# Performance work log

Measured on AMD Instinct MI355X. Metric: run time of the kernel, lower is better.

Reference implementation:

```python
import jax, jax.numpy as jnp
import numpy as np

L, E, H, FF, N, S, ML = 6, 768, 12, 3072, 8, 1023, 2048


def setup_inputs() -> dict:
    key = jax.random.key(0)
    ks = jax.random.split(key, 16)
    rn = lambda k, shape, s=0.02: jax.random.normal(k, shape, jnp.float32) * s
    return {
        "x": jax.random.normal(ks[0], (N, S, E), jnp.float32),
        "mask": jnp.ones((N, 1, 1, S + 1), jnp.int32),
        "pos_emb": rn(ks[1], (ML, E), 1.0),
        "cls": rn(ks[2], (1, 1, E), 1.0),
        "Wq": rn(ks[3], (L, E, E)), "bq": jnp.zeros((L, E), jnp.float32),
        "Wk": rn(ks[4], (L, E, E)), "bk": jnp.zeros((L, E), jnp.float32),
        "Wv": rn(ks[5], (L, E, E)), "bv": jnp.zeros((L, E), jnp.float32),
        "Wo": rn(ks[6], (L, E, E)), "bo": jnp.zeros((L, E), jnp.float32),
        "ln1_g": jnp.ones((L, E), jnp.float32), "ln1_b": jnp.zeros((L, E), jnp.float32),
        "ln2_g": jnp.ones((L, E), jnp.float32), "ln2_b": jnp.zeros((L, E), jnp.float32),
        "Wf1": rn(ks[7], (L, E, FF)), "bf1": jnp.zeros((L, FF), jnp.float32),
        "Wf2": rn(ks[8], (L, FF, E)), "bf2": jnp.zeros((L, E), jnp.float32),
    }


def _ln(x, g, b, eps=1e-5):
    m = x.mean(-1, keepdims=True)
    v = ((x - m) ** 2).mean(-1, keepdims=True)
    return (x - m) / jnp.sqrt(v + eps) * g + b


def reference(x, mask, pos_emb, cls, Wq, bq, Wk, bk, Wv, bv, Wo, bo,
              ln1_g, ln1_b, ln2_g, ln2_b, Wf1, bf1, Wf2, bf2):
    n, s, e = x.shape
    h = H
    d = e // h
    # prepend CLS token -> [N, T, E], add learned positions
    x = jnp.concatenate([jnp.broadcast_to(cls, (n, 1, e)), x], axis=1)
    t = s + 1
    out = x + pos_emb[:t][None]
    scale = jnp.float32(1.0 / np.sqrt(d))
    for i in range(Wq.shape[0]):
        q = (out @ Wq[i] + bq[i]).reshape(n, t, h, d)
        k = (out @ Wk[i] + bk[i]).reshape(n, t, h, d)
        v = (out @ Wv[i] + bv[i]).reshape(n, t, h, d)
        energy = jnp.einsum('nqhd,nkhd->nhqk', q, k)  # [N,H,T,T]
        energy = jnp.where(mask == 0, jnp.float32(-1e20), energy)
        attn = jax.nn.softmax(energy * scale, axis=-1)
        att = jnp.einsum('nhqk,nkhd->nqhd', attn, v).reshape(n, t, e)
        att = att @ Wo[i] + bo[i]
        hid = _ln(att + out, ln1_g[i], ln1_b[i])  # residual uses query (=out)
        ff = jax.nn.gelu(hid @ Wf1[i] + bf1[i], approximate=False) @ Wf2[i] + bf2[i]
        out = _ln(ff + hid, ln2_g[i], ln2_b[i])
    return out
```

## Files before the change

### kernel.cpp

```cpp
#include <hip/hip_runtime.h>

#define L_ 6
#define E_ 768
#define H_ 12
#define FF_ 3072

typedef __attribute__((ext_vector_type(8))) short bh8;
typedef __attribute__((ext_vector_type(4))) float f32x4;

__device__ inline ushort f2bf(float f) {
  unsigned u = __builtin_bit_cast(unsigned, f);
  u += 0x7fffu + ((u >> 16) & 1u);
  return (ushort)(u >> 16);
}

__device__ __forceinline__ void gload16(const void* g, void* l) {
  __builtin_amdgcn_global_load_lds(
      (const __attribute__((address_space(1))) void*)g,
      (__attribute__((address_space(3))) void*)l, 16, 0, 0);
}

__global__ __launch_bounds__(256) void pack_bias(const float* __restrict__ bq,
                                                 const float* __restrict__ bk,
                                                 const float* __restrict__ bv,
                                                 float* __restrict__ bqkv) {
  int idx = blockIdx.x * 256 + threadIdx.x;
  int l = idx / 2304, j = idx % 2304;
  float v = (j < 768) ? bq[l * 768 + j]
          : (j < 1536) ? bk[l * 768 + j - 768]
                       : bv[l * 768 + j - 1536];
  bqkv[idx] = v;
}

__global__ __launch_bounds__(256) void transpose_w(const float* __restrict__ src,
                                                   ushort* __restrict__ dst,
                                                   int K, int Nn,
                                                   long sstride, long dstride) {
  src += (long)blockIdx.z * sstride;
  dst += (long)blockIdx.z * dstride;
  __shared__ float t[32][33];
  int tx = threadIdx.x & 31, ty = threadIdx.x >> 5;
  int kb = blockIdx.x * 32, nb = blockIdx.y * 32;
#pragma unroll
  for (int i = 0; i < 4; i++) {
    int kr = ty + i * 8;
    t[kr][tx] = src[(long)(kb + kr) * Nn + nb + tx];
  }
  __syncthreads();
#pragma unroll
  for (int i = 0; i < 4; i++) {
    int nr = ty + i * 8;
    dst[(long)(nb + nr) * K + kb + tx] = f2bf(t[tx][nr]);
  }
}

__global__ __launch_bounds__(256) void embed_k(const float* __restrict__ x,
                                               const float* __restrict__ pos,
                                               const float* __restrict__ cls,
                                               float* __restrict__ res,
                                               ushort* __restrict__ xb) {
  int idx = blockIdx.x * 256 + threadIdx.x;
  int c4 = idx % 192;
  int row = idx / 192;
  int t = row & 1023, n = row >> 10;
  f32x4 pv = ((const f32x4*)pos)[t * 192 + c4];
  f32x4 xv;
  if (t == 0) xv = ((const f32x4*)cls)[c4];
  else        xv = ((const f32x4*)x)[(size_t)(n * 1023 + t - 1) * 192 + c4];
  f32x4 s = xv + pv;
  ((f32x4*)res)[idx] = s;
  ushort4 h;
  h.x = f2bf(s[0]); h.y = f2bf(s[1]); h.z = f2bf(s[2]); h.w = f2bf(s[3]);
  ((ushort4*)xb)[idx] = h;
}

template <int MODE>
__global__ __launch_bounds__(256) void gemm_bt(const ushort* __restrict__ A,
                                               const ushort* __restrict__ Bt,
                                               int M, int N, int K,
                                               const float* __restrict__ bias,
                                               const float* __restrict__ resid,
                                               float* __restrict__ out32,
                                               ushort* __restrict__ out16,
                                               ushort* __restrict__ vtb) {
  __shared__ ushort As[3][128 * 32];
  __shared__ ushort Bs[3][128 * 32];
  int tid = threadIdx.x;
  int wid = tid >> 6, lane = tid & 63;
  int wm = wid >> 1, wn = wid & 1;
  int l15 = lane & 15, lhi = lane >> 4;
  int ln4 = lane >> 2;
  int swc = (((lane & 3) ^ (ln4 & 3)) << 3);
  int xsl = ((lhi ^ (l15 & 3)) << 3);
  int row0 = blockIdx.x * 128, col0 = blockIdx.y * 128;

  f32x4 acc[4][4];
#pragma unroll
  for (int i = 0; i < 4; i++)
#pragma unroll
    for (int j = 0; j < 4; j++) acc[i][j] = (f32x4){0.f, 0.f, 0.f, 0.f};

  const ushort* Ab = A + (size_t)(row0 + wid * 32 + ln4) * K + swc;
  const ushort* Bb = Bt + (size_t)(col0 + wid * 32 + ln4) * K + swc;

  auto stage = [&](int b, int kt) {
#pragma unroll
    for (int it = 0; it < 2; ++it) {
      int r = wid * 32 + it * 16;
      gload16(Ab + (size_t)it * 16 * K + kt * 32, &As[b][r * 32]);
      gload16(Bb + (size_t)it * 16 * K + kt * 32, &Bs[b][r * 32]);
    }
  };

  int nt = K >> 5;
  stage(0, 0);
  stage(1, 1);
  int b0 = 0;
  for (int kt = 0; kt < nt; ++kt) {
    int rem = nt - kt;
    if (rem > 2) {
      stage((b0 + 2 >= 3) ? b0 - 1 : b0 + 2, kt + 2);
      asm volatile("s_waitcnt vmcnt(8)" ::: "memory");
    } else if (rem == 2) {
      asm volatile("s_waitcnt vmcnt(4)" ::: "memory");
    } else {
      asm volatile("s_waitcnt vmcnt(0)" ::: "memory");
    }
    __builtin_amdgcn_s_barrier();

    bh8 af[4], bfr[4];
#pragma unroll
    for (int i = 0; i < 4; i++)
      af[i] = *(const bh8*)(&As[b0][(wm * 64 + i * 16 + l15) * 32 + xsl]);
#pragma unroll
    for (int j = 0; j < 4; j++)
      bfr[j] = *(const bh8*)(&Bs[b0][(wn * 64 + j * 16 + l15) * 32 + xsl]);
#pragma unroll
    for (int i = 0; i < 4; i++)
#pragma unroll
      for (int j = 0; j < 4; j++)
        acc[i][j] = __builtin_amdgcn_mfma_f32_16x16x32_bf16(af[i], bfr[j], acc[i][j], 0, 0, 0);

    if (rem > 1) {
      asm volatile("s_waitcnt lgkmcnt(0)" ::: "memory");
      __builtin_amdgcn_s_barrier();
    }
    b0 = (b0 + 1 == 3) ? 0 : b0 + 1;
  }

#pragma unroll
  for (int j = 0; j < 4; j++) {
    int col = col0 + wn * 64 + j * 16 + l15;
    float bv = bias[col];
#pragma unroll
    for (int i = 0; i < 4; i++) {
      int rbase = row0 + wm * 64 + i * 16 + lhi * 4;
      if (MODE == 0 && col >= 1536) {
        int hd = col - 1536;
        int nn = rbase >> 10, t0 = rbase & 1023;
        ushort4 h4;
        h4.x = f2bf(acc[i][j][0] + bv);
        h4.y = f2bf(acc[i][j][1] + bv);
        h4.z = f2bf(acc[i][j][2] + bv);
        h4.w = f2bf(acc[i][j][3] + bv);
        *(ushort4*)(vtb + ((size_t)nn * 768 + hd) * 1024 + t0) = h4;
      } else {
#pragma unroll
        for (int r = 0; r < 4; r++) {
          int row = rbase + r;
          size_t o = (size_t)row * N + col;
          float v = acc[i][j][r] + bv;
          if (MODE == 0) {
            out16[o] = f2bf(v);
          } else if (MODE == 1) {
            out32[o] = v + resid[o];
          } else {
            v = 0.5f * v * (1.f + erff(v * 0.70710678118f));
            out16[o] = f2bf(v);
          }
        }
      }
    }
  }
}

__global__ __launch_bounds__(256) void attn_k(const ushort* __restrict__ qkv,
                                              const ushort* __restrict__ vtb,
                                              const int* __restrict__ mask,
                                              ushort* __restrict__ attb) {
  int qt = blockIdx.x, h = blockIdx.y, n = blockIdx.z;
  int tid = threadIdx.x, wid = tid >> 6, lane = tid & 63;
  int l15 = lane & 15, lhi = lane >> 4;
  __shared__ ushort Ks[2][64 * 64];
  __shared__ ushort Vs[2][64 * 64];
  __shared__ ushort Pt[4][16 * 64];
  ushort* Pw = Pt[wid];

  int ln8 = lane >> 3;
  int swc = (((lane & 7) ^ ln8) << 3);

  const ushort* Kg = qkv + 768 + h * 64;
  const ushort* Vg = vtb + (size_t)(n * 768 + h * 64) * 1024;

  auto stage = [&](int b, int kv0) {
#pragma unroll
    for (int it = 0; it < 2; ++it) {
      int r = wid * 16 + it * 8;
      gload16(Kg + (size_t)(n * 1024 + kv0 + r + ln8) * 2304 + swc, &Ks[b][r * 64]);
      gload16(Vg + (size_t)(r + ln8) * 1024 + kv0 + swc, &Vs[b][r * 64]);
    }
  };

  stage(0, 0);

  int q0 = qt * 64 + wid * 16;
  size_t rowQ = (size_t)(n * 1024 + q0 + l15) * 2304 + h * 64;
  bh8 qf0 = *(const bh8*)(qkv + rowQ + lhi * 8);
  bh8 qf1 = *(const bh8*)(qkv + rowQ + 32 + lhi * 8);

  unsigned long long mbits = 0ull;
#pragma unroll
  for (int i = 0; i < 64; ++i)
    mbits |= (unsigned long long)(mask[n * 1024 + i * 16 + l15] != 0) << i;

  bh8 ones;
#pragma unroll
  for (int i = 0; i < 8; ++i) ones[i] = (short)0x3F80;

  f32x4 o[4], lacc = (f32x4){0.f, 0.f, 0.f, 0.f};
#pragma unroll
  for (int i = 0; i < 4; i++) o[i] = (f32x4){0.f, 0.f, 0.f, 0.f};

  int x15 = (l15 & 7) << 3;
  int buf = 0;
  for (int t = 0; t < 16; ++t) {
    if (t < 15) {
      stage(buf ^ 1, (t + 1) * 64);
      asm volatile("s_waitcnt vmcnt(4)" ::: "memory");
    } else {
      asm volatile("s_waitcnt vmcnt(0)" ::: "memory");
    }
    __builtin_amdgcn_s_barrier();
    const ushort* Kb = Ks[buf];
    const ushort* Vb = Vs[buf];

    f32x4 s[4];
    __builtin_amdgcn_s_setprio(1);
#pragma unroll
    for (int t4 = 0; t4 < 4; ++t4) {
      int rs = (t4 * 16 + l15) * 64;
      s[t4] = (f32x4){0.f, 0.f, 0.f, 0.f};
      s[t4] = __builtin_amdgcn_mfma_f32_16x16x32_bf16(qf0, *(const bh8*)(Kb + rs + ((lhi << 3) ^ x15)), s[t4], 0, 0, 0);
      s[t4] = __builtin_amdgcn_mfma_f32_16x16x32_bf16(qf1, *(const bh8*)(Kb + rs + (((4 + lhi) << 3) ^ x15)), s[t4], 0, 0, 0);
    }
    __builtin_amdgcn_s_setprio(0);

#pragma unroll
    for (int t4 = 0; t4 < 4; ++t4) {
      bool mk = (mbits >> (t * 4 + t4)) & 1ull;
#pragma unroll
      for (int r = 0; r < 4; r++) {
        float xv = mk ? s[t4][r] * 0.125f : -1e20f;
        float p = __expf(fminf(xv, 80.f));
        int prow = lhi * 4 + r;
        int slot = t4 * 2 + (l15 >> 3);
        Pw[prow * 64 + (((slot ^ (prow & 7)) << 3) | (l15 & 7))] = f2bf(p);
      }
    }

    bh8 pf0 = *(const bh8*)(Pw + l15 * 64 + ((lhi << 3) ^ x15));
    bh8 pf1 = *(const bh8*)(Pw + l15 * 64 + (((4 + lhi) << 3) ^ x15));
    __builtin_amdgcn_s_setprio(1);
#pragma unroll
    for (int nb = 0; nb < 4; nb++) {
      int rs = (nb * 16 + l15) * 64;
      o[nb] = __builtin_amdgcn_mfma_f32_16x16x32_bf16(pf0, *(const bh8*)(Vb + rs + ((lhi << 3) ^ x15)), o[nb], 0, 0, 0);
      o[nb] = __builtin_amdgcn_mfma_f32_16x16x32_bf16(pf1, *(const bh8*)(Vb + rs + (((4 + lhi) << 3) ^ x15)), o[nb], 0, 0, 0);
    }
    lacc = __builtin_amdgcn_mfma_f32_16x16x32_bf16(pf0, ones, lacc, 0, 0, 0);
    lacc = __builtin_amdgcn_mfma_f32_16x16x32_bf16(pf1, ones, lacc, 0, 0, 0);
    __builtin_amdgcn_s_setprio(0);

    if (t < 15) {
      asm volatile("s_waitcnt lgkmcnt(0)" ::: "memory");
      __builtin_amdgcn_s_barrier();
    }
    buf ^= 1;
  }

#pragma unroll
  for (int nb = 0; nb < 4; nb++)
#pragma unroll
    for (int r = 0; r < 4; r++) {
      float val = o[nb][r] / lacc[r];
      int row = q0 + lhi * 4 + r;
      int col = h * 64 + nb * 16 + l15;
      attb[(size_t)(n * 1024 + row) * 768 + col] = f2bf(val);
    }
}

__global__ __launch_bounds__(256) void ln_k(const float* __restrict__ in,
                                            const float* __restrict__ g,
                                            const float* __restrict__ b,
                                            float* __restrict__ y32,
                                            ushort* __restrict__ y16) {
  int row = blockIdx.x, tid = threadIdx.x;
  size_t base = (size_t)row * 768;
  float v0 = in[base + tid], v1 = in[base + tid + 256], v2 = in[base + tid + 512];
  float s = v0 + v1 + v2;
  float sq = v0 * v0 + v1 * v1 + v2 * v2;
#pragma unroll
  for (int off = 32; off > 0; off >>= 1) {
    s += __shfl_down(s, off);
    sq += __shfl_down(sq, off);
  }
  __shared__ float sws[4], swq[4];
  int wid = tid >> 6, lane = tid & 63;
  if (lane == 0) { sws[wid] = s; swq[wid] = sq; }
  __syncthreads();
  float ts = sws[0] + sws[1] + sws[2] + sws[3];
  float tq = swq[0] + swq[1] + swq[2] + swq[3];
  float mean = ts * (1.f / 768.f);
  float var = tq * (1.f / 768.f) - mean * mean;
  float rstd = rsqrtf(var + 1e-5f);
#pragma unroll
  for (int i = 0; i < 3; i++) {
    int c = tid + i * 256;
    float vv = (i == 0) ? v0 : (i == 1) ? v1 : v2;
    float y = (vv - mean) * rstd * g[c] + b[c];
    y32[base + c] = y;
    y16[base + c] = f2bf(y);
  }
}

extern "C" void kernel_launch(void* const* d_in, const int* in_sizes, int n_in,
                              void* d_out, int out_size, void* d_ws, size_t ws_size,
                              hipStream_t stream) {
  const float* x    = (const float*)d_in[0];
  const int*   mask = (const int*)d_in[1];
  const float* pos  = (const float*)d_in[2];
  const float* cls  = (const float*)d_in[3];
  const float* Wq   = (const float*)d_in[4];
  const float* bq   = (const float*)d_in[5];
  const float* Wk   = (const float*)d_in[6];
  const float* bk   = (const float*)d_in[7];
  const float* Wv   = (const float*)d_in[8];
  const float* bv   = (const float*)d_in[9];
  const float* Wo   = (const float*)d_in[10];
  const float* bo   = (const float*)d_in[11];
  const float* ln1g = (const float*)d_in[12];
  const float* ln1b = (const float*)d_in[13];
  const float* ln2g = (const float*)d_in[14];
  const float* ln2b = (const float*)d_in[15];
  const float* Wf1  = (const float*)d_in[16];
  const float* bf1  = (const float*)d_in[17];
  const float* Wf2  = (const float*)d_in[18];
  const float* bf2  = (const float*)d_in[19];

  char* ws = (char*)d_ws;
  size_t off = 0;
  auto alloc = [&](size_t bytes) {
    char* p = ws + off;
    off += (bytes + 255) & ~(size_t)255;
    return p;
  };
  const size_t M = 8192;
  ushort* qkvt = (ushort*)alloc((size_t)L_ * 2304 * 768 * 2);
  ushort* wot  = (ushort*)alloc((size_t)L_ * 768 * 768 * 2);
  ushort* wf1t = (ushort*)alloc((size_t)L_ * 3072 * 768 * 2);
  ushort* wf2t = (ushort*)alloc((size_t)L_ * 768 * 3072 * 2);
  float*  bqkv = (float*)alloc((size_t)L_ * 2304 * 4);
  float*  res  = (float*)alloc(M * 768 * 4);
  float*  pre  = (float*)alloc(M * 768 * 4);
  ushort* xb   = (ushort*)alloc(M * 768 * 2);
  ushort* qkvb = (ushort*)alloc(M * 2304 * 2);
  ushort* vtb  = (ushort*)alloc(M * 768 * 2);
  ushort* attb = (ushort*)alloc(M * 768 * 2);
  ushort* ffb  = (ushort*)alloc(M * 3072 * 2);
  (void)ws_size; (void)in_sizes; (void)n_in; (void)out_size;

  dim3 tb(256);
  pack_bias<<<54, tb, 0, stream>>>(bq, bk, bv, bqkv);
  transpose_w<<<dim3(24, 24, 6), tb, 0, stream>>>(Wq, qkvt,              768, 768, 768L * 768, 2304L * 768);
  transpose_w<<<dim3(24, 24, 6), tb, 0, stream>>>(Wk, qkvt + 768 * 768,  768, 768, 768L * 768, 2304L * 768);
  transpose_w<<<dim3(24, 24, 6), tb, 0, stream>>>(Wv, qkvt + 2 * 768 * 768, 768, 768, 768L * 768, 2304L * 768);
  transpose_w<<<dim3(24, 24, 6), tb, 0, stream>>>(Wo, wot, 768, 768, 768L * 768, 768L * 768);
  transpose_w<<<dim3(24, 96, 6), tb, 0, stream>>>(Wf1, wf1t, 768, 3072, 768L * 3072, 3072L * 768);
  transpose_w<<<dim3(96, 24, 6), tb, 0, stream>>>(Wf2, wf2t, 3072, 768, 3072L * 768, 768L * 3072);
  embed_k<<<6144, tb, 0, stream>>>(x, pos, cls, res, xb);

  for (int l = 0; l < L_; l++) {
    gemm_bt<0><<<dim3(64, 18), tb, 0, stream>>>(xb, qkvt + (size_t)l * 2304 * 768,
                                                8192, 2304, 768, bqkv + l * 2304,
                                                nullptr, nullptr, qkvb, vtb);
    attn_k<<<dim3(16, 12, 8), tb, 0, stream>>>(qkvb, vtb, mask, attb);
    gemm_bt<1><<<dim3(64, 6), tb, 0, stream>>>(attb, wot + (size_t)l * 768 * 768,
                                               8192, 768, 768, bo + l * 768,
                                               res, pre, nullptr, nullptr);
    ln_k<<<8192, tb, 0, stream>>>(pre, ln1g + l * 768, ln1b + l * 768, res, xb);
    gemm_bt<2><<<dim3(64, 24), tb, 0, stream>>>(xb, wf1t + (size_t)l * 3072 * 768,
                                                8192, 3072, 768, bf1 + l * 3072,
                                                nullptr, nullptr, ffb, nullptr);
    gemm_bt<1><<<dim3(64, 6), tb, 0, stream>>>(ffb, wf2t + (size_t)l * 768 * 3072,
                                               8192, 768, 3072, bf2 + l * 768,
                                               res, pre, nullptr, nullptr);
    float* y32 = (l == L_ - 1) ? (float*)d_out : res;
    ln_k<<<8192, tb, 0, stream>>>(pre, ln2g + l * 768, ln2b + l * 768, y32, xb);
  }
}
```

Measured before the change: 1.976 ms.

## Replace triple-buffered GEMM pipeline with single-buffer BK=64 loop and higher occupancy

The GEMM main loop drops its 3-stage software-pipelined LDS ring with manual vmcnt waits. It now uses a single LDS buffer with K-tile 64, loads and computes each tile synchronously between __syncthreads, and sets launch_bounds to 4 blocks per CU. The XOR swizzle on LDS addresses is removed. Latency hiding now depends on occupancy instead of in-block prefetch. The unswizzled 128-byte row stride may cause LDS bank conflicts on the fragment reads.

```diff
diff --git a/kernel.cpp b/kernel.cpp
--- a/kernel.cpp
+++ b/kernel.cpp
@@ -75,23 +75,21 @@
 }
 
 template <int MODE>
-__global__ __launch_bounds__(256) void gemm_bt(const ushort* __restrict__ A,
-                                               const ushort* __restrict__ Bt,
-                                               int M, int N, int K,
-                                               const float* __restrict__ bias,
-                                               const float* __restrict__ resid,
-                                               float* __restrict__ out32,
-                                               ushort* __restrict__ out16,
-                                               ushort* __restrict__ vtb) {
-  __shared__ ushort As[3][128 * 32];
-  __shared__ ushort Bs[3][128 * 32];
+__global__ __launch_bounds__(256, 4) void gemm_bt(const ushort* __restrict__ A,
+                                                  const ushort* __restrict__ Bt,
+                                                  int M, int N, int K,
+                                                  const float* __restrict__ bias,
+                                                  const float* __restrict__ resid,
+                                                  float* __restrict__ out32,
+                                                  ushort* __restrict__ out16,
+                                                  ushort* __restrict__ vtb) {
+  __shared__ ushort As[128 * 64];
+  __shared__ ushort Bs[128 * 64];
   int tid = threadIdx.x;
   int wid = tid >> 6, lane = tid & 63;
   int wm = wid >> 1, wn = wid & 1;
   int l15 = lane & 15, lhi = lane >> 4;
-  int ln4 = lane >> 2;
-  int swc = (((lane & 3) ^ (ln4 & 3)) << 3);
-  int xsl = ((lhi ^ (l15 & 3)) << 3);
+  int ln8 = lane >> 3, lc8 = (lane & 7) * 8;
   int row0 = blockIdx.x * 128, col0 = blockIdx.y * 128;
 
   f32x4 acc[4][4];
@@ -100,52 +98,35 @@
 #pragma unroll
     for (int j = 0; j < 4; j++) acc[i][j] = (f32x4){0.f, 0.f, 0.f, 0.f};
 
-  const ushort* Ab = A + (size_t)(row0 + wid * 32 + ln4) * K + swc;
-  const ushort* Bb = Bt + (size_t)(col0 + wid * 32 + ln4) * K + swc;
-
-  auto stage = [&](int b, int kt) {
-#pragma unroll
-    for (int it = 0; it < 2; ++it) {
-      int r = wid * 32 + it * 16;
-      gload16(Ab + (size_t)it * 16 * K + kt * 32, &As[b][r * 32]);
-      gload16(Bb + (size_t)it * 16 * K + kt * 32, &Bs[b][r * 32]);
-    }
-  };
-
-  int nt = K >> 5;
-  stage(0, 0);
-  stage(1, 1);
-  int b0 = 0;
+  const ushort* Ap = A + (size_t)(row0 + wid * 32 + ln8) * K + lc8;
+  const ushort* Bp = Bt + (size_t)(col0 + wid * 32 + ln8) * K + lc8;
+
+  int nt = K >> 6;
   for (int kt = 0; kt < nt; ++kt) {
-    int rem = nt - kt;
-    if (rem > 2) {
-      stage((b0 + 2 >= 3) ? b0 - 1 : b0 + 2, kt + 2);
-      asm volatile("s_waitcnt vmcnt(8)" ::: "memory");
-    } else if (rem == 2) {
-      asm volatile("s_waitcnt vmcnt(4)" ::: "memory");
-    } else {
-      asm volatile("s_waitcnt vmcnt(0)" ::: "memory");
-    }
-    __builtin_amdgcn_s_barrier();
-
-    bh8 af[4], bfr[4];
-#pragma unroll
-    for (int i = 0; i < 4; i++)
-      af[i] = *(const bh8*)(&As[b0][(wm * 64 + i * 16 + l15) * 32 + xsl]);
-#pragma unroll
-    for (int j = 0; j < 4; j++)
-      bfr[j] = *(const bh8*)(&Bs[b0][(wn * 64 + j * 16 + l15) * 32 + xsl]);
-#pragma unroll
-    for (int i = 0; i < 4; i++)
+    int k0 = kt << 6;
+#pragma unroll
+    for (int p = 0; p < 4; p++) {
+      int r = wid * 32 + p * 8;
+      gload16(Ap + (size_t)p * 8 * K + k0, As + r * 64);
+      gload16(Bp + (size_t)p * 8 * K + k0, Bs + r * 64);
+    }
+    __syncthreads();
+#pragma unroll
+    for (int ks = 0; ks < 2; ks++) {
+      bh8 af[4], bfr[4];
+#pragma unroll
+      for (int i = 0; i < 4; i++)
+        af[i] = *(const bh8*)(As + (wm * 64 + i * 16 + l15) * 64 + ks * 32 + lhi * 8);
 #pragma unroll
       for (int j = 0; j < 4; j++)
-        acc[i][j] = __builtin_amdgcn_mfma_f32_16x16x32_bf16(af[i], bfr[j], acc[i][j], 0, 0, 0);
-
-    if (rem > 1) {
-      asm volatile("s_waitcnt lgkmcnt(0)" ::: "memory");
-      __builtin_amdgcn_s_barrier();
-    }
-    b0 = (b0 + 1 == 3) ? 0 : b0 + 1;
+        bfr[j] = *(const bh8*)(Bs + (wn * 64 + j * 16 + l15) * 64 + ks * 32 + lhi * 8);
+#pragma unroll
+      for (int i = 0; i < 4; i++)
+#pragma unroll
+        for (int j = 0; j < 4; j++)
+          acc[i][j] = __builtin_amdgcn_mfma_f32_16x16x32_bf16(af[i], bfr[j], acc[i][j], 0, 0, 0);
+    }
+    __syncthreads();
   }
 
 #pragma unroll
```

After: 2.028 ms. +2.6%, slower.
